# Optimization experiments

Measured on AMD Instinct MI355X. Metric: run time of the kernel, lower is better.

## Reference

```python
import jax, jax.numpy as jnp
import numpy as np

L, D, H, DK, DV, DFF = 6, 512, 8, 64, 64, 2048
B, S = 8, 512
EPS = 1e-5


def _pos_table(max_len, d_model):
    pos = np.arange(max_len)[:, None].astype(np.float64)
    i = np.arange(d_model)[None, :].astype(np.float64)
    t = pos / np.power(10000.0, 2.0 * i / d_model)
    t[0, :] = 0.0
    t[1:, 0::2] = np.sin(t[1:, 0::2])
    t[1:, 1::2] = np.cos(t[1:, 1::2])
    return jnp.asarray(t, dtype=jnp.float32)


def _ln(x, g, b):
    m = jnp.mean(x, axis=-1, keepdims=True)
    v = jnp.mean(jnp.square(x - m), axis=-1, keepdims=True)
    return (x - m) * jax.lax.rsqrt(v + EPS) * g + b


def setup_inputs() -> dict:
    key = jax.random.key(0)
    ks = jax.random.split(key, 12)
    s = 0.02
    return {
        "enc_inputs": jax.random.normal(ks[0], (B, S, D), jnp.float32),
        "enc_inputs_mask": jax.random.randint(ks[1], (B, S), 0, 100, dtype=jnp.int64),
        "Wq": jax.random.normal(ks[2], (L, D, H * DK), jnp.float32) * s,
        "Wk": jax.random.normal(ks[3], (L, D, H * DK), jnp.float32) * s,
        "Wv": jax.random.normal(ks[4], (L, D, H * DV), jnp.float32) * s,
        "Wo": jax.random.normal(ks[5], (L, H * DV, D), jnp.float32) * s,
        "ln1_g": jnp.ones((L, D), jnp.float32),
        "ln1_b": jnp.zeros((L, D), jnp.float32),
        "W1": jax.random.normal(ks[6], (L, D, DFF), jnp.float32) * s,
        "W2": jax.random.normal(ks[7], (L, DFF, D), jnp.float32) * s,
        "ln2_g": jnp.ones((L, D), jnp.float32),
        "ln2_b": jnp.zeros((L, D), jnp.float32),
    }


def reference(enc_inputs, enc_inputs_mask, Wq, Wk, Wv, Wo, ln1_g, ln1_b, W1, W2, ln2_g, ln2_b):
    b, s, _ = enc_inputs.shape
    x = enc_inputs + _pos_table(s, D)  # positional encoding (dropout = eval/no-op)
    # pad mask: True where key token is pad (mask id == 0); broadcast over heads & queries
    pad = (enc_inputs_mask == 0)[:, None, None, :]  # [B,1,1,S]
    inv_sqrt_dk = np.float32(1.0 / np.sqrt(DK))
    attns = []
    for l in range(L):
        residual = x
        q = (x @ Wq[l]).reshape(b, s, H, DK).transpose(0, 2, 1, 3)  # [B,H,S,DK]
        k = (x @ Wk[l]).reshape(b, s, H, DK).transpose(0, 2, 1, 3)
        v = (x @ Wv[l]).reshape(b, s, H, DV).transpose(0, 2, 1, 3)
        scores = jnp.einsum("bhqd,bhkd->bhqk", q, k) * inv_sqrt_dk
        scores = jnp.where(pad, jnp.float32(-1e9), scores)
        attn = jax.nn.softmax(scores, axis=-1)
        ctx = jnp.einsum("bhqk,bhkd->bhqd", attn, v)
        ctx = ctx.transpose(0, 2, 1, 3).reshape(b, s, H * DV)
        x = _ln(ctx @ Wo[l] + residual, ln1_g[l], ln1_b[l])
        x = _ln(jax.nn.relu(x @ W1[l]) @ W2[l] + x, ln2_g[l], ln2_b[l])
        attns.append(attn)
    return x, jnp.stack(attns)  # [B,S,D], [L,B,H,S,S]
```

## Files before the change

### kernel.cpp

```cpp
#include <hip/hip_runtime.h>

typedef __attribute__((ext_vector_type(8))) short bf16x8;
typedef __attribute__((ext_vector_type(4))) short bf16x4;
typedef __attribute__((ext_vector_type(4))) float f32x4;

__device__ __forceinline__ float b2f(ushort u) {
  union { uint u; float f; } x; x.u = ((uint)u) << 16; return x.f;
}
__device__ __forceinline__ ushort f2b(float f) {
  union { float f; uint u; } x; x.f = f;
  uint r = x.u + 0x7fffu + ((x.u >> 16) & 1u);
  return (ushort)(r >> 16);
}
__device__ __forceinline__ f32x4 mfma16(bf16x8 a, bf16x8 b, f32x4 c) {
  return __builtin_amdgcn_mfma_f32_16x16x32_bf16(a, b, c, 0, 0, 0);
}
__device__ __forceinline__ void glds16(const ushort* g, ushort* l) {
  __builtin_amdgcn_global_load_lds((const __attribute__((address_space(1))) void*)g,
                                   (__attribute__((address_space(3))) void*)l, 16, 0, 0);
}

__global__ void detect_kernel(const uint* __restrict__ ln1g, const uint* __restrict__ mask,
                              int* __restrict__ flags) {
  if (threadIdx.x == 0) {
    flags[0] = (ln1g[0] == 0x3F800000u) ? 1 : 0;
    int odd0 = 1;
    for (int i = 0; i < 16; i++)
      if (mask[2 * i + 1] != 0u) odd0 = 0;
    flags[1] = odd0;
  }
}

__global__ __launch_bounds__(256) void convt_kernel(const void* __restrict__ src,
                                                    ushort* __restrict__ dst, int K, int N,
                                                    const int* __restrict__ flags) {
  __shared__ ushort T[64][72];
  int f = flags[0];
  size_t mo = (size_t)blockIdx.z * K * N;
  int k0 = blockIdx.x * 64, n0 = blockIdx.y * 64;
  int r = threadIdx.x >> 2, c = (threadIdx.x & 3) * 16;
  if (f) {
    const float* sp = (const float*)src + mo + (size_t)(k0 + r) * N + n0 + c;
#pragma unroll
    for (int i = 0; i < 16; i += 4) {
      float4 fv = *(const float4*)(sp + i);
      T[c + i][r] = f2b(fv.x); T[c + i + 1][r] = f2b(fv.y);
      T[c + i + 2][r] = f2b(fv.z); T[c + i + 3][r] = f2b(fv.w);
    }
  } else {
    const ushort* sp = (const ushort*)src + mo + (size_t)(k0 + r) * N + n0 + c;
    bf16x8 v0 = *(const bf16x8*)sp;
    bf16x8 v1 = *(const bf16x8*)(sp + 8);
#pragma unroll
    for (int i = 0; i < 8; i++) { T[c + i][r] = (ushort)v0[i]; T[c + 8 + i][r] = (ushort)v1[i]; }
  }
  __syncthreads();
  ushort* d = dst + mo + (size_t)(n0 + r) * K + k0 + c;
  *(bf16x8*)d = *(const bf16x8*)&T[r][c];
  *(bf16x8*)(d + 8) = *(const bf16x8*)&T[r][c + 8];
}

__global__ __launch_bounds__(256) void posadd_kernel(const void* __restrict__ enc,
                                                     float* __restrict__ x32,
                                                     ushort* __restrict__ xb,
                                                     const int* __restrict__ flags) {
  int f = flags[0];
  int idx = blockIdx.x * 256 + threadIdx.x;
  int s = idx >> 9, d = idx & 511;
  float pef = 0.f;
  if (s > 0) {
    double t = (double)s / pow(10000.0, 2.0 * (double)d / 512.0);
    pef = (float)((d & 1) ? cos(t) : sin(t));
  }
  for (int b = 0; b < 8; b++) {
    size_t o = ((size_t)(b * 512 + s)) * 512 + d;
    float ev = f ? ((const float*)enc)[o] : b2f(((const ushort*)enc)[o]);
    float xv = ev + pef;
    x32[o] = xv;
    xb[o] = f2b(xv);
  }
}

template <bool RELU, int OUTMODE>
__device__ __forceinline__ void gemm_bt_core(const ushort* __restrict__ A,
                                             const ushort* __restrict__ Bt,
                                             ushort* __restrict__ C,
                                             int M, int N, int K, int bm, int bn) {
  __shared__ ushort As[128 * 64];
  __shared__ ushort Bs[128 * 64];
  int tid = threadIdx.x;
  int wave = tid >> 6, lane = tid & 63;
  int lm = lane & 15, lq = lane >> 4;
  int wm = (wave & 1) * 64, wn = (wave >> 1) * 64;
  int m0 = bm * 128, n0 = bn * 128;
  f32x4 z = {0.f, 0.f, 0.f, 0.f};
  f32x4 acc[4][4];
#pragma unroll
  for (int mi = 0; mi < 4; mi++)
#pragma unroll
    for (int ni = 0; ni < 4; ni++) acc[mi][ni] = z;

  int sr = tid >> 3, sc = (tid & 7) * 8;
  const ushort* ap = A + (size_t)(m0 + sr) * K + sc;
  const ushort* bp = Bt + (size_t)(n0 + sr) * K + sc;
  ushort* asd = As + tid * 8;
  ushort* bsd = Bs + tid * 8;

  for (int k0 = 0; k0 < K; k0 += 64) {
#pragma unroll
    for (int j = 0; j < 4; j++) {
      glds16(ap + (size_t)(j * 32) * K + k0, asd + j * 2048);
      glds16(bp + (size_t)(j * 32) * K + k0, bsd + j * 2048);
    }
    __syncthreads();
#pragma unroll
    for (int kk = 0; kk < 64; kk += 32) {
      bf16x8 af[4], bfv[4];
#pragma unroll
      for (int mi = 0; mi < 4; mi++)
        af[mi] = *(const bf16x8*)&As[(wm + mi * 16 + lm) * 64 + kk + lq * 8];
#pragma unroll
      for (int ni = 0; ni < 4; ni++)
        bfv[ni] = *(const bf16x8*)&Bs[(wn + ni * 16 + lm) * 64 + kk + lq * 8];
#pragma unroll
      for (int mi = 0; mi < 4; mi++)
#pragma unroll
        for (int ni = 0; ni < 4; ni++)
          acc[mi][ni] = mfma16(af[mi], bfv[ni], acc[mi][ni]);
    }
    __syncthreads();
  }

  if (OUTMODE == 0) {
#pragma unroll
    for (int mi = 0; mi < 4; mi++)
#pragma unroll
      for (int ni = 0; ni < 4; ni++) {
        int row = m0 + wm + mi * 16 + lq * 4;
        int col = n0 + wn + ni * 16 + lm;
#pragma unroll
        for (int r = 0; r < 4; r++) {
          float vv = acc[mi][ni][r];
          if (RELU) vv = fmaxf(vv, 0.f);
          C[(size_t)(row + r) * N + col] = f2b(vv);
        }
      }
  } else {
#pragma unroll
    for (int mi = 0; mi < 4; mi++)
#pragma unroll
      for (int ni = 0; ni < 4; ni++) {
        int row = m0 + wm + mi * 16 + lq * 4;
        int col = n0 + wn + ni * 16 + lm;
        int b = row >> 9, s = row & 511;
        bf16x4 o;
#pragma unroll
        for (int r = 0; r < 4; r++) o[r] = (short)f2b(acc[mi][ni][r]);
        *(bf16x4*)&C[((size_t)(b * 8 + (col >> 6)) * 64 + (col & 63)) * 512 + s] = o;
      }
  }
}

template <bool RELU>
__global__ __launch_bounds__(256) void gemm_bt_kernel(const ushort* __restrict__ A,
                                                      const ushort* __restrict__ Bt,
                                                      ushort* __restrict__ C, int M, int N, int K) {
  gemm_bt_core<RELU, 0>(A, Bt, C, M, N, K, blockIdx.x, blockIdx.y);
}

__global__ __launch_bounds__(256) void gemm_qkv_kernel(const ushort* __restrict__ A,
                                                       const ushort* __restrict__ Wq,
                                                       const ushort* __restrict__ Wk,
                                                       const ushort* __restrict__ Wv,
                                                       ushort* __restrict__ q, ushort* __restrict__ k,
                                                       ushort* __restrict__ vt, int M, int N, int K) {
  if (blockIdx.z == 0)      gemm_bt_core<false, 0>(A, Wq, q,  M, N, K, blockIdx.x, blockIdx.y);
  else if (blockIdx.z == 1) gemm_bt_core<false, 0>(A, Wk, k,  M, N, K, blockIdx.x, blockIdx.y);
  else                      gemm_bt_core<false, 1>(A, Wv, vt, M, N, K, blockIdx.x, blockIdx.y);
}

__global__ __launch_bounds__(256) void attn_kernel(const ushort* __restrict__ qb, const ushort* __restrict__ kb,
                                                   const ushort* __restrict__ vt, const uint* __restrict__ mask,
                                                   void* __restrict__ out_base, size_t out_elem_off,
                                                   ushort* __restrict__ ctx, const int* __restrict__ flags) {
  __shared__ float Sc[16][516];
  __shared__ ushort Pb[16][520];
  __shared__ ushort Qs[16][72];
  __shared__ float red[16][16];
  __shared__ float rowmax[16];
  __shared__ float rowrinv[16];
  int of32 = flags[0], m64 = flags[1];
  int tid = threadIdx.x, wave = tid >> 6, lane = tid & 63;
  int lm = lane & 15, lq = lane >> 4;
  int bh = blockIdx.x, b = bh >> 3, h = bh & 7;
  int q0 = blockIdx.y * 16;
  {
    int r = tid >> 4, c = (tid & 15) * 4;
    const ushort* src = qb + (size_t)(b * 512 + q0 + r) * 512 + h * 64 + c;
    *(bf16x4*)&Qs[r][c] = *(const bf16x4*)src;
  }
  __syncthreads();
  bf16x8 a0 = *(const bf16x8*)&Qs[lm][lq * 8];
  bf16x8 a1 = *(const bf16x8*)&Qs[lm][32 + lq * 8];
  f32x4 z = {0.f, 0.f, 0.f, 0.f};
  for (int t8 = 0; t8 < 8; t8++) {
    int key = (wave * 8 + t8) * 16 + lm;
    const ushort* kp = kb + (size_t)(b * 512 + key) * 512 + h * 64;
    bf16x8 kb0 = *(const bf16x8*)(kp + lq * 8);
    bf16x8 kb1 = *(const bf16x8*)(kp + 32 + lq * 8);
    f32x4 s = mfma16(a0, kb0, z);
    s = mfma16(a1, kb1, s);
    uint mv = mask[(size_t)(b * 512 + key) << m64];
#pragma unroll
    for (int r = 0; r < 4; r++) {
      Sc[lq * 4 + r][key] = (mv == 0u) ? -1e9f : s[r] * 0.125f;
    }
  }
  __syncthreads();
  int row = tid >> 4, seg = tid & 15;
  float mx = -3.0e38f;
  for (int i = 0; i < 32; i++) {
    int ii = seg * 32 + ((i + seg * 2) & 31);
    mx = fmaxf(mx, Sc[row][ii]);
  }
  red[row][seg] = mx;
  __syncthreads();
  if (seg == 0) {
    float m = red[row][0];
    for (int i = 1; i < 16; i++) m = fmaxf(m, red[row][i]);
    rowmax[row] = m;
  }
  __syncthreads();
  float rmax = rowmax[row];
  float sum = 0.f;
  for (int i = 0; i < 32; i++) {
    int ii = seg * 32 + ((i + seg * 2) & 31);
    float e = expf(Sc[row][ii] - rmax);
    Sc[row][ii] = e;
    sum += e;
  }
  red[row][seg] = sum;
  __syncthreads();
  if (seg == 0) {
    float t = 0.f;
    for (int i = 0; i < 16; i++) t += red[row][i];
    rowrinv[row] = 1.f / t;
  }
  __syncthreads();
  float rinv = rowrinv[row];
  size_t rowbase = out_elem_off + ((size_t)(b * 8 + h) * 512 + (q0 + row)) * 512;
#pragma unroll
  for (int io = 0; io < 4; io++) {
    int ch = seg * 32 + (((io + seg) & 3) * 8);
    float pf[8];
    bf16x8 pv;
#pragma unroll
    for (int j = 0; j < 8; j++) {
      pf[j] = Sc[row][ch + j] * rinv;
      pv[j] = (short)f2b(pf[j]);
    }
    *(bf16x8*)&Pb[row][ch] = pv;
    if (of32) {
      float* ao = (float*)out_base;
      float4 p0 = {pf[0], pf[1], pf[2], pf[3]};
      float4 p1 = {pf[4], pf[5], pf[6], pf[7]};
      *(float4*)(ao + rowbase + ch) = p0;
      *(float4*)(ao + rowbase + ch + 4) = p1;
    } else {
      *(bf16x8*)((ushort*)out_base + rowbase + ch) = pv;
    }
  }
  __syncthreads();
  f32x4 c = z;
  int d = wave * 16 + lm;
  const ushort* vp = vt + ((size_t)bh * 64 + d) * 512;
#pragma unroll 4
  for (int ks = 0; ks < 16; ks++) {
    bf16x8 ap = *(const bf16x8*)&Pb[lm][ks * 32 + lq * 8];
    bf16x8 bv = *(const bf16x8*)(vp + ks * 32 + lq * 8);
    c = mfma16(ap, bv, c);
  }
#pragma unroll
  for (int r = 0; r < 4; r++) {
    ctx[(size_t)(b * 512 + q0 + lq * 4 + r) * 512 + h * 64 + d] = f2b(c[r]);
  }
}

__global__ __launch_bounds__(256) void ln_kernel(const ushort* __restrict__ a, float* __restrict__ x32,
                                                 ushort* __restrict__ xb, const void* __restrict__ g,
                                                 const void* __restrict__ bb, int goff,
                                                 const int* __restrict__ flags) {
  int f = flags[0];
  int row = blockIdx.x, tid = threadIdx.x;
  size_t base = (size_t)row * 512;
  float v0 = b2f(a[base + tid]) + x32[base + tid];
  float v1 = b2f(a[base + tid + 256]) + x32[base + tid + 256];
  float s1 = v0 + v1, s2 = v0 * v0 + v1 * v1;
#pragma unroll
  for (int off = 32; off > 0; off >>= 1) {
    s1 += __shfl_down(s1, off);
    s2 += __shfl_down(s2, off);
  }
  __shared__ float r1[4], r2[4];
  if ((tid & 63) == 0) { r1[tid >> 6] = s1; r2[tid >> 6] = s2; }
  __syncthreads();
  s1 = r1[0] + r1[1] + r1[2] + r1[3];
  s2 = r2[0] + r2[1] + r2[2] + r2[3];
  float m = s1 * (1.f / 512.f);
  float var = s2 * (1.f / 512.f) - m * m;
  float rs = rsqrtf(var + 1e-5f);
  float g0, g1v, b0, b1;
  if (f) {
    const float* gp = (const float*)g + goff;
    const float* bp = (const float*)bb + goff;
    g0 = gp[tid]; g1v = gp[tid + 256]; b0 = bp[tid]; b1 = bp[tid + 256];
  } else {
    const ushort* gp = (const ushort*)g + goff;
    const ushort* bp = (const ushort*)bb + goff;
    g0 = b2f(gp[tid]); g1v = b2f(gp[tid + 256]); b0 = b2f(bp[tid]); b1 = b2f(bp[tid + 256]);
  }
  float y0 = (v0 - m) * rs * g0 + b0;
  float y1 = (v1 - m) * rs * g1v + b1;
  x32[base + tid] = y0;        xb[base + tid] = f2b(y0);
  x32[base + tid + 256] = y1;  xb[base + tid + 256] = f2b(y1);
}

__global__ __launch_bounds__(256) void outx_kernel(const float* __restrict__ x32, void* __restrict__ out,
                                                   const int* __restrict__ flags) {
  int f = flags[0];
  int i = (blockIdx.x * 256 + threadIdx.x) * 4;
  float4 v = *(const float4*)(x32 + i);
  if (f) {
    *(float4*)((float*)out + i) = v;
  } else {
    bf16x4 o;
    o[0] = (short)f2b(v.x); o[1] = (short)f2b(v.y); o[2] = (short)f2b(v.z); o[3] = (short)f2b(v.w);
    *(bf16x4*)((ushort*)out + i) = o;
  }
}

extern "C" void kernel_launch(void* const* d_in, const int* in_sizes, int n_in,
                              void* d_out, int out_size, void* d_ws, size_t ws_size,
                              hipStream_t stream) {
  const void* enc  = d_in[0];
  const uint* mask = (const uint*)d_in[1];
  const void* Wq   = d_in[2];
  const void* Wk   = d_in[3];
  const void* Wv   = d_in[4];
  const void* Wo   = d_in[5];
  const void* ln1g = d_in[6];
  const void* ln1b = d_in[7];
  const void* W1   = d_in[8];
  const void* W2   = d_in[9];
  const void* ln2g = d_in[10];
  const void* ln2b = d_in[11];

  char* p = (char*)d_ws;
  int* flags  = (int*)p;      p += 256;
  ushort* tWq = (ushort*)p;   p += (size_t)1572864 * 2;
  ushort* tWk = (ushort*)p;   p += (size_t)1572864 * 2;
  ushort* tWv = (ushort*)p;   p += (size_t)1572864 * 2;
  ushort* tWo = (ushort*)p;   p += (size_t)1572864 * 2;
  ushort* tW1 = (ushort*)p;   p += (size_t)6291456 * 2;
  ushort* tW2 = (ushort*)p;   p += (size_t)6291456 * 2;
  float*  x32 = (float*)p;    p += (size_t)2097152 * 4;
  ushort* xb  = (ushort*)p;   p += (size_t)2097152 * 2;
  ushort* g2  = (ushort*)p;   p += (size_t)2097152 * 2;
  ushort* ctx = (ushort*)p;   p += (size_t)2097152 * 2;
  ushort* q   = (ushort*)p;   p += (size_t)2097152 * 2;
  ushort* k   = (ushort*)p;   p += (size_t)2097152 * 2;
  p += (size_t)2097152 * 2;
  ushort* vt  = (ushort*)p;   p += (size_t)2097152 * 2;
  ushort* g1  = q;

  detect_kernel<<<1, 64, 0, stream>>>((const uint*)ln1g, mask, flags);
  convt_kernel<<<dim3(8, 8, 6),  256, 0, stream>>>(Wq, tWq, 512, 512, flags);
  convt_kernel<<<dim3(8, 8, 6),  256, 0, stream>>>(Wk, tWk, 512, 512, flags);
  convt_kernel<<<dim3(8, 8, 6),  256, 0, stream>>>(Wv, tWv, 512, 512, flags);
  convt_kernel<<<dim3(8, 8, 6),  256, 0, stream>>>(Wo, tWo, 512, 512, flags);
  convt_kernel<<<dim3(8, 32, 6), 256, 0, stream>>>(W1, tW1, 512, 2048, flags);
  convt_kernel<<<dim3(32, 8, 6), 256, 0, stream>>>(W2, tW2, 2048, 512, flags);
  posadd_kernel<<<1024, 256, 0, stream>>>(enc, x32, xb, flags);

  for (int l = 0; l < 6; l++) {
    gemm_qkv_kernel<<<dim3(32, 4, 3), 256, 0, stream>>>(
        xb, tWq + (size_t)l * 262144, tWk + (size_t)l * 262144, tWv + (size_t)l * 262144,
        q, k, vt, 4096, 512, 512);
    attn_kernel<<<dim3(64, 32), 256, 0, stream>>>(
        q, k, vt, mask, d_out, (size_t)2097152 + (size_t)l * 16777216, ctx, flags);
    gemm_bt_kernel<false><<<dim3(32, 4), 256, 0, stream>>>(ctx, tWo + (size_t)l * 262144, g2, 4096, 512, 512);
    ln_kernel<<<4096, 256, 0, stream>>>(g2, x32, xb, ln1g, ln1b, l * 512, flags);
    gemm_bt_kernel<true><<<dim3(32, 16), 256, 0, stream>>>(xb, tW1 + (size_t)l * 1048576, g1, 4096, 2048, 512);
    gemm_bt_kernel<false><<<dim3(32, 4), 256, 0, stream>>>(g1, tW2 + (size_t)l * 1048576, g2, 4096, 512, 2048);
    ln_kernel<<<4096, 256, 0, stream>>>(g2, x32, xb, ln2g, ln2b, l * 512, flags);
  }
  outx_kernel<<<2048, 256, 0, stream>>>(x32, d_out, flags);
}
```

Baseline: 1.396 ms.

## Double-buffer GEMM LDS loads, register-resident softmax, and fuse weight conversions

The GEMM core now uses two LDS buffers, so the next K tile is prefetched while the current one is multiplied, with one barrier per iteration instead of two. The attention kernel keeps scores in registers, reduces max and sum with wave shuffles plus a small cross-wave LDS step, precomputes the pad mask in LDS, and writes P through an XOR-swizzled buffer. The six weight transpose/convert launches are merged into one kernel. The trade-offs are double the GEMM LDS use, which may lower occupancy, and attention probability stores that are now scalar per element rather than vectorised rows.

```diff
diff --git a/kernel.cpp b/kernel.cpp
--- a/kernel.cpp
+++ b/kernel.cpp
@@ -19,6 +19,7 @@
   __builtin_amdgcn_global_load_lds((const __attribute__((address_space(1))) void*)g,
                                    (__attribute__((address_space(3))) void*)l, 16, 0, 0);
 }
+#define VMCNT0 asm volatile("s_waitcnt vmcnt(0)" ::: "memory")
 
 __global__ void detect_kernel(const uint* __restrict__ ln1g, const uint* __restrict__ mask,
                               int* __restrict__ flags) {
@@ -31,13 +32,10 @@
   }
 }
 
-__global__ __launch_bounds__(256) void convt_kernel(const void* __restrict__ src,
-                                                    ushort* __restrict__ dst, int K, int N,
-                                                    const int* __restrict__ flags) {
+__device__ __forceinline__ void convt_tile(const void* __restrict__ src, ushort* __restrict__ dst,
+                                           int K, int N, int l, int k0, int n0, int f) {
   __shared__ ushort T[64][72];
-  int f = flags[0];
-  size_t mo = (size_t)blockIdx.z * K * N;
-  int k0 = blockIdx.x * 64, n0 = blockIdx.y * 64;
+  size_t mo = (size_t)l * K * N;
   int r = threadIdx.x >> 2, c = (threadIdx.x & 3) * 16;
   if (f) {
     const float* sp = (const float*)src + mo + (size_t)(k0 + r) * N + n0 + c;
@@ -58,6 +56,33 @@
   ushort* d = dst + mo + (size_t)(n0 + r) * K + k0 + c;
   *(bf16x8*)d = *(const bf16x8*)&T[r][c];
   *(bf16x8*)(d + 8) = *(const bf16x8*)&T[r][c + 8];
+}
+
+__global__ __launch_bounds__(256) void convt_all_kernel(
+    const void* __restrict__ Wq, const void* __restrict__ Wk, const void* __restrict__ Wv,
+    const void* __restrict__ Wo, const void* __restrict__ W1, const void* __restrict__ W2,
+    ushort* __restrict__ tWq, ushort* __restrict__ tWk, ushort* __restrict__ tWv,
+    ushort* __restrict__ tWo, ushort* __restrict__ tW1, ushort* __restrict__ tW2,
+    const int* __restrict__ flags) {
+  int f = flags[0];
+  int id = blockIdx.x;
+  if (id < 1536) {
+    const void* s; ushort* d;
+    if (id < 384)       { s = Wq; d = tWq; }
+    else if (id < 768)  { s = Wk; d = tWk; id -= 384; }
+    else if (id < 1152) { s = Wv; d = tWv; id -= 768; }
+    else                { s = Wo; d = tWo; id -= 1152; }
+    int l = id >> 6, rr = id & 63;
+    convt_tile(s, d, 512, 512, l, (rr & 7) * 64, (rr >> 3) * 64, f);
+  } else if (id < 3072) {
+    int r = id - 1536;
+    int l = r >> 8, rr = r & 255;
+    convt_tile(W1, tW1, 512, 2048, l, (rr & 7) * 64, (rr >> 3) * 64, f);
+  } else {
+    int r = id - 3072;
+    int l = r >> 8, rr = r & 255;
+    convt_tile(W2, tW2, 2048, 512, l, (rr & 31) * 64, (rr >> 5) * 64, f);
+  }
 }
 
 __global__ __launch_bounds__(256) void posadd_kernel(const void* __restrict__ enc,
@@ -86,8 +111,8 @@
                                              const ushort* __restrict__ Bt,
                                              ushort* __restrict__ C,
                                              int M, int N, int K, int bm, int bn) {
-  __shared__ ushort As[128 * 64];
-  __shared__ ushort Bs[128 * 64];
+  __shared__ ushort As[2 * 128 * 64];
+  __shared__ ushort Bs[2 * 128 * 64];
   int tid = threadIdx.x;
   int wave = tid >> 6, lane = tid & 63;
   int lm = lane & 15, lq = lane >> 4;
@@ -103,32 +128,46 @@
   int sr = tid >> 3, sc = (tid & 7) * 8;
   const ushort* ap = A + (size_t)(m0 + sr) * K + sc;
   const ushort* bp = Bt + (size_t)(n0 + sr) * K + sc;
-  ushort* asd = As + tid * 8;
-  ushort* bsd = Bs + tid * 8;
-
-  for (int k0 = 0; k0 < K; k0 += 64) {
-#pragma unroll
-    for (int j = 0; j < 4; j++) {
-      glds16(ap + (size_t)(j * 32) * K + k0, asd + j * 2048);
-      glds16(bp + (size_t)(j * 32) * K + k0, bsd + j * 2048);
+  int nt = K >> 6;
+
+#pragma unroll
+  for (int j = 0; j < 4; j++) {
+    glds16(ap + (size_t)(j * 32) * K, As + tid * 8 + j * 2048);
+    glds16(bp + (size_t)(j * 32) * K, Bs + tid * 8 + j * 2048);
+  }
+  VMCNT0;
+  __builtin_amdgcn_s_barrier();
+  __builtin_amdgcn_sched_barrier(0);
+
+  for (int t = 0; t < nt; t++) {
+    int cur = (t & 1) * 8192;
+    if (t + 1 < nt) {
+      int nxt = ((t + 1) & 1) * 8192;
+      int k0 = (t + 1) << 6;
+#pragma unroll
+      for (int j = 0; j < 4; j++) {
+        glds16(ap + (size_t)(j * 32) * K + k0, As + nxt + tid * 8 + j * 2048);
+        glds16(bp + (size_t)(j * 32) * K + k0, Bs + nxt + tid * 8 + j * 2048);
+      }
     }
-    __syncthreads();
 #pragma unroll
     for (int kk = 0; kk < 64; kk += 32) {
       bf16x8 af[4], bfv[4];
 #pragma unroll
       for (int mi = 0; mi < 4; mi++)
-        af[mi] = *(const bf16x8*)&As[(wm + mi * 16 + lm) * 64 + kk + lq * 8];
+        af[mi] = *(const bf16x8*)&As[cur + (wm + mi * 16 + lm) * 64 + kk + lq * 8];
 #pragma unroll
       for (int ni = 0; ni < 4; ni++)
-        bfv[ni] = *(const bf16x8*)&Bs[(wn + ni * 16 + lm) * 64 + kk + lq * 8];
+        bfv[ni] = *(const bf16x8*)&Bs[cur + (wn + ni * 16 + lm) * 64 + kk + lq * 8];
 #pragma unroll
       for (int mi = 0; mi < 4; mi++)
 #pragma unroll
         for (int ni = 0; ni < 4; ni++)
           acc[mi][ni] = mfma16(af[mi], bfv[ni], acc[mi][ni]);
     }
-    __syncthreads();
+    VMCNT0;
+    __builtin_amdgcn_s_barrier();
+    __builtin_amdgcn_sched_barrier(0);
   }
 
   if (OUTMODE == 0) {
@@ -183,12 +222,11 @@
                                                    const ushort* __restrict__ vt, const uint* __restrict__ mask,
                                                    void* __restrict__ out_base, size_t out_elem_off,
                                                    ushort* __restrict__ ctx, const int* __restrict__ flags) {
-  __shared__ float Sc[16][516];
-  __shared__ ushort Pb[16][520];
   __shared__ ushort Qs[16][72];
-  __shared__ float red[16][16];
-  __shared__ float rowmax[16];
-  __shared__ float rowrinv[16];
+  __shared__ float maskf[512];
+  __shared__ float redm[4][16];
+  __shared__ float reds[4][16];
+  __shared__ ushort Pb[16 * 512];
   int of32 = flags[0], m64 = flags[1];
   int tid = threadIdx.x, wave = tid >> 6, lane = tid & 63;
   int lm = lane & 15, lq = lane >> 4;
@@ -199,10 +237,20 @@
     const ushort* src = qb + (size_t)(b * 512 + q0 + r) * 512 + h * 64 + c;
     *(bf16x4*)&Qs[r][c] = *(const bf16x4*)src;
   }
+  if (tid < 256) {
+#pragma unroll
+    for (int i = 0; i < 2; i++) {
+      int kk = tid * 2 + i;
+      uint mv = mask[(size_t)(b * 512 + kk) << m64];
+      maskf[kk] = (mv == 0u) ? -1e9f : 0.f;
+    }
+  }
   __syncthreads();
   bf16x8 a0 = *(const bf16x8*)&Qs[lm][lq * 8];
   bf16x8 a1 = *(const bf16x8*)&Qs[lm][32 + lq * 8];
   f32x4 z = {0.f, 0.f, 0.f, 0.f};
+  f32x4 acc[8];
+#pragma unroll
   for (int t8 = 0; t8 < 8; t8++) {
     int key = (wave * 8 + t8) * 16 + lm;
     const ushort* kp = kb + (size_t)(b * 512 + key) * 512 + h * 64;
@@ -210,65 +258,81 @@
     bf16x8 kb1 = *(const bf16x8*)(kp + 32 + lq * 8);
     f32x4 s = mfma16(a0, kb0, z);
     s = mfma16(a1, kb1, s);
-    uint mv = mask[(size_t)(b * 512 + key) << m64];
-#pragma unroll
-    for (int r = 0; r < 4; r++) {
-      Sc[lq * 4 + r][key] = (mv == 0u) ? -1e9f : s[r] * 0.125f;
+    float mf = maskf[key];
+#pragma unroll
+    for (int r = 0; r < 4; r++) acc[t8][r] = s[r] * 0.125f + mf;
+  }
+  float rmax[4];
+#pragma unroll
+  for (int r = 0; r < 4; r++) {
+    float v = acc[0][r];
+#pragma unroll
+    for (int t8 = 1; t8 < 8; t8++) v = fmaxf(v, acc[t8][r]);
+    v = fmaxf(v, __shfl_xor(v, 1));
+    v = fmaxf(v, __shfl_xor(v, 2));
+    v = fmaxf(v, __shfl_xor(v, 4));
+    v = fmaxf(v, __shfl_xor(v, 8));
+    rmax[r] = v;
+  }
+  if (lm == 0) {
+#pragma unroll
+    for (int r = 0; r < 4; r++) redm[wave][lq * 4 + r] = rmax[r];
+  }
+  __syncthreads();
+#pragma unroll
+  for (int r = 0; r < 4; r++) {
+    int row = lq * 4 + r;
+    rmax[r] = fmaxf(fmaxf(redm[0][row], redm[1][row]), fmaxf(redm[2][row], redm[3][row]));
+  }
+  float rsum[4];
+#pragma unroll
+  for (int r = 0; r < 4; r++) {
+    float s = 0.f;
+#pragma unroll
+    for (int t8 = 0; t8 < 8; t8++) {
+      float e = expf(acc[t8][r] - rmax[r]);
+      acc[t8][r] = e;
+      s += e;
     }
-  }
-  __syncthreads();
-  int row = tid >> 4, seg = tid & 15;
-  float mx = -3.0e38f;
-  for (int i = 0; i < 32; i++) {
-    int ii = seg * 32 + ((i + seg * 2) & 31);
-    mx = fmaxf(mx, Sc[row][ii]);
-  }
-  red[row][seg] = mx;
-  __syncthreads();
-  if (seg == 0) {
-    float m = red[row][0];
-    for (int i = 1; i < 16; i++) m = fmaxf(m, red[row][i]);
-    rowmax[row] = m;
-  }
-  __syncthreads();
-  float rmax = rowmax[row];
-  float sum = 0.f;
-  for (int i = 0; i < 32; i++) {
-    int ii = seg * 32 + ((i + seg * 2) & 31);
-    float e = expf(Sc[row][ii] - rmax);
-    Sc[row][ii] = e;
-    sum += e;
-  }
-  red[row][seg] = sum;
-  __syncthreads();
-  if (seg == 0) {
-    float t = 0.f;
-    for (int i = 0; i < 16; i++) t += red[row][i];
-    rowrinv[row] = 1.f / t;
-  }
-  __syncthreads();
-  float rinv = rowrinv[row];
-  size_t rowbase = out_elem_off + ((size_t)(b * 8 + h) * 512 + (q0 + row)) * 512;
-#pragma unroll
-  for (int io = 0; io < 4; io++) {
-    int ch = seg * 32 + (((io + seg) & 3) * 8);
-    float pf[8];
-    bf16x8 pv;
-#pragma unroll
-    for (int j = 0; j < 8; j++) {
-      pf[j] = Sc[row][ch + j] * rinv;
-      pv[j] = (short)f2b(pf[j]);
-    }
-    *(bf16x8*)&Pb[row][ch] = pv;
-    if (of32) {
-      float* ao = (float*)out_base;
-      float4 p0 = {pf[0], pf[1], pf[2], pf[3]};
-      float4 p1 = {pf[4], pf[5], pf[6], pf[7]};
-      *(float4*)(ao + rowbase + ch) = p0;
-      *(float4*)(ao + rowbase + ch + 4) = p1;
-    } else {
-      *(bf16x8*)((ushort*)out_base + rowbase + ch) = pv;
-    }
+    s += __shfl_xor(s, 1);
+    s += __shfl_xor(s, 2);
+    s += __shfl_xor(s, 4);
+    s += __shfl_xor(s, 8);
+    rsum[r] = s;
+  }
+  if (lm == 0) {
+#pragma unroll
+    for (int r = 0; r < 4; r++) reds[wave][lq * 4 + r] = rsum[r];
+  }
+  __syncthreads();
+  float rinv[4];
+#pragma unroll
+  for (int r = 0; r < 4; r++) {
+    int row = lq * 4 + r;
+    rinv[r] = 1.f / (reds[0][row] + reds[1][row] + reds[2][row] + reds[3][row]);
+  }
+  if (of32) {
+    float* ao = (float*)out_base;
+#pragma unroll
+    for (int t8 = 0; t8 < 8; t8++)
+#pragma unroll
+      for (int r = 0; r < 4; r++) {
+        int row = lq * 4 + r, key = (wave * 8 + t8) * 16 + lm;
+        float pf = acc[t8][r] * rinv[r];
+        Pb[(row * 512 + key) ^ ((row & 7) << 3)] = f2b(pf);
+        ao[out_elem_off + ((size_t)(b * 8 + h) * 512 + q0 + row) * 512 + key] = pf;
+      }
+  } else {
+    ushort* ao = (ushort*)out_base;
+#pragma unroll
+    for (int t8 = 0; t8 < 8; t8++)
+#pragma unroll
+      for (int r = 0; r < 4; r++) {
+        int row = lq * 4 + r, key = (wave * 8 + t8) * 16 + lm;
+        ushort pb = f2b(acc[t8][r] * rinv[r]);
+        Pb[(row * 512 + key) ^ ((row & 7) << 3)] = pb;
+        ao[out_elem_off + ((size_t)(b * 8 + h) * 512 + q0 + row) * 512 + key] = pb;
+      }
   }
   __syncthreads();
   f32x4 c = z;
@@ -276,9 +340,9 @@
   const ushort* vp = vt + ((size_t)bh * 64 + d) * 512;
 #pragma unroll 4
   for (int ks = 0; ks < 16; ks++) {
-    bf16x8 ap = *(const bf16x8*)&Pb[lm][ks * 32 + lq * 8];
+    bf16x8 pa = *(const bf16x8*)&Pb[(lm * 512 + ks * 32 + lq * 8) ^ ((lm & 7) << 3)];
     bf16x8 bv = *(const bf16x8*)(vp + ks * 32 + lq * 8);
-    c = mfma16(ap, bv, c);
+    c = mfma16(pa, bv, c);
   }
 #pragma unroll
   for (int r = 0; r < 4; r++) {
@@ -374,12 +438,8 @@
   ushort* g1  = q;
 
   detect_kernel<<<1, 64, 0, stream>>>((const uint*)ln1g, mask, flags);
-  convt_kernel<<<dim3(8, 8, 6),  256, 0, stream>>>(Wq, tWq, 512, 512, flags);
-  convt_kernel<<<dim3(8, 8, 6),  256, 0, stream>>>(Wk, tWk, 512, 512, flags);
-  convt_kernel<<<dim3(8, 8, 6),  256, 0, stream>>>(Wv, tWv, 512, 512, flags);
-  convt_kernel<<<dim3(8, 8, 6),  256, 0, stream>>>(Wo, tWo, 512, 512, flags);
-  convt_kernel<<<dim3(8, 32, 6), 256, 0, stream>>>(W1, tW1, 512, 2048, flags);
-  convt_kernel<<<dim3(32, 8, 6), 256, 0, stream>>>(W2, tW2, 2048, 512, flags);
+  convt_all_kernel<<<4608, 256, 0, stream>>>(Wq, Wk, Wv, Wo, W1, W2,
+                                             tWq, tWk, tWv, tWo, tW1, tW2, flags);
   posadd_kernel<<<1024, 256, 0, stream>>>(enc, x32, xb, flags);
 
   for (int l = 0; l < 6; l++) {
```

Result: faster. 1.367 ms (-2.1%).
